# Performance work log

Measured on AMD Instinct MI355X. Metric: run time of the kernel, lower is better.

## Reference

```python
import jax, jax.numpy as jnp
import numpy as np

G = 4          # conv groups (hardcoded in module)
C = 1024       # channels (hardcoded cin=cout=1024)
SCALE = 1.0 / np.sqrt(1024.0).astype(np.float32)  # 1/sqrt(c/h), h=1


def grouped_proj(x, W, b):
    # pointwise grouped Conv1d == block-diagonal matmul over channel groups
    # x: [B, C, P], W: [G, C//G out, C//G in], b: [C]
    B, C_, P = x.shape
    xg = x.reshape(B, G, C_ // G, P)
    y = jnp.einsum('goi,bgip->bgop', W, xg)  # [B, G, C//G, P]
    return y.reshape(B, C_, P) + b[None, :, None]


def setup_inputs() -> dict:
    key = jax.random.key(0)
    ks = jax.random.split(key, 8)
    B, PK, PQ = 8, 1024, 4096
    cg = C // G
    w_std = 1.0 / np.sqrt(cg).astype(np.float32)  # ~ conv default init scale
    return {
        'Xq': jax.random.normal(ks[0], (B, C, PQ), jnp.float32),
        'Xk': jax.random.normal(ks[1], (B, C, PK), jnp.float32),
        'Wq': jax.random.normal(ks[2], (G, cg, cg), jnp.float32) * w_std,
        'bq': jax.random.normal(ks[3], (C,), jnp.float32) * 0.01,
        'Wk': jax.random.normal(ks[4], (G, cg, cg), jnp.float32) * w_std,
        'bk': jax.random.normal(ks[5], (C,), jnp.float32) * 0.01,
        'Wv': jax.random.normal(ks[6], (G, cg, cg), jnp.float32) * w_std,
        'bv': jax.random.normal(ks[7], (C,), jnp.float32) * 0.01,
    }


def reference(Xq, Xk, Wq, bq, Wk, bk, Wv, bv):
    # Q and K are both projected from Xk; V from Xq (as in the torch code)
    Q = grouped_proj(Xk, Wq, bq)   # [B, C, Pk]
    K = grouped_proj(Xk, Wk, bk)   # [B, C, Pk]
    V = grouped_proj(Xq, Wv, bv)   # [B, C, Pq]
    b, c, pk = K.shape
    pq = V.shape[-1]
    h = 1
    Qh = Q.reshape(b, h, c // h, pk)
    Kh = K.reshape(b, h, c // h, pk)
    Vh = V.reshape(b, h, c // h, pq)
    # H: [B, h, Pk, Pq], contraction over channels; softmax over dim=-2 (Pk)
    H = jnp.einsum('bhci,bhcj->bhij', Kh, Vh) * SCALE
    H = jax.nn.softmax(H, axis=-2)
    # sparse_constrain: Gram over last axis vs identity, mean squared error
    mid = jnp.einsum('bhci,bhki->bhck', H, H)          # [B, h, Pk, Pk]
    Iden = jnp.eye(pk, dtype=H.dtype)[None, None]       # broadcast over B, h
    sparse_loss = jnp.mean((mid - Iden) ** 2)
    # out: mix Q along Pk with attention H -> [B, h, C, Pq]
    out = jnp.einsum('bhij,bhki->bhkj', H, Qh).reshape(b, c, pq)
    return out, sparse_loss, H
```

## Files before the change

kernel.cpp:

```cpp
#include <hip/hip_runtime.h>

typedef _Float16 f16;
typedef f16 f16x4 __attribute__((ext_vector_type(4)));
typedef f16 f16x8 __attribute__((ext_vector_type(8)));
typedef float f32x4 __attribute__((ext_vector_type(4)));

__device__ __forceinline__ void gload16(const void* g, void* ldsbase) {
  __builtin_amdgcn_global_load_lds((const __attribute__((address_space(1))) unsigned int*)g,
                                   (__attribute__((address_space(3))) unsigned int*)ldsbase, 16, 0, 0);
}

__device__ __forceinline__ int swz(int row, int c) {
  return row * 64 + ((c ^ ((row >> 1) & 3)) << 4);
}

template<int MODE>
__global__ void __launch_bounds__(512, 2)
gemm256(const f16* __restrict__ A, const f16* __restrict__ Bm, float* __restrict__ Cf,
        f16* __restrict__ E16, f16* __restrict__ E16t,
        int K, long sA, long sB, float scale, float* __restrict__ aux) {
  __shared__ f16 sb[65536];
  const int t = threadIdx.x, l = t & 63, w = t >> 6;
  const int wr = w >> 2, wc = w & 3;
  const int bid = blockIdx.x;
  const int swzb = (bid & 7) * 64 + (bid >> 3);
  const long b = swzb >> 6;
  const int inner = swzb & 63;
  const int bx = inner >> 2, by = inner & 3;
  const char* Abyte = (const char*)(A + b * sA + (long)(by * 256) * K);
  const char* Bbyte = (const char*)(Bm + b * sB + (long)(bx * 256) * K);

  int offSrc[4];
#pragma unroll
  for (int i = 0; i < 4; ++i) {
    int cid = i * 512 + t, row = cid >> 3, slot = cid & 7;
    offSrc[i] = row * (K * 2) + ((slot ^ (row & 7)) << 4);
  }
  int offAf[8][2], offBf[4][2];
#pragma unroll
  for (int mi = 0; mi < 8; ++mi) {
    int r = wr * 128 + mi * 16 + (l & 15);
#pragma unroll
    for (int ks = 0; ks < 2; ++ks)
      offAf[mi][ks] = r * 64 + ((((ks << 2) + (l >> 4)) ^ (r & 7)) << 3);
  }
#pragma unroll
  for (int ni = 0; ni < 4; ++ni) {
    int r = wc * 64 + ni * 16 + (l & 15);
#pragma unroll
    for (int ks = 0; ks < 2; ++ks)
      offBf[ni][ks] = r * 64 + ((((ks << 2) + (l >> 4)) ^ (r & 7)) << 3);
  }

  const int NT = K >> 6;
  f32x4 acc[8][4] = {};

  auto STAGE = [&](int kt, int bsel) {
    f16* la = sb + bsel * 32768;
    f16* lb = la + 16384;
    const char* as = Abyte + (long)kt * 128;
    const char* bs = Bbyte + (long)kt * 128;
#pragma unroll
    for (int i = 0; i < 4; ++i)
      gload16(as + offSrc[i], la + (i * 512 + (w << 6)) * 8);
#pragma unroll
    for (int i = 0; i < 4; ++i)
      gload16(bs + offSrc[i], lb + (i * 512 + (w << 6)) * 8);
  };

  STAGE(0, 0);
  for (int kt = 0; kt < NT; ++kt) {
    const int cur = kt & 1;
    if (kt + 1 < NT) {
      STAGE(kt + 1, cur ^ 1);
      asm volatile("s_waitcnt vmcnt(8)" ::: "memory");
    } else {
      asm volatile("s_waitcnt vmcnt(0)" ::: "memory");
    }
    __builtin_amdgcn_s_barrier();
    asm volatile("" ::: "memory");
    const f16* la = sb + cur * 32768;
    const f16* lb = la + 16384;
#pragma unroll
    for (int ks = 0; ks < 2; ++ks) {
      f16x8 bf[4];
#pragma unroll
      for (int ni = 0; ni < 4; ++ni) bf[ni] = *(const f16x8*)(lb + offBf[ni][ks]);
#pragma unroll
      for (int mi = 0; mi < 8; ++mi) {
        f16x8 af = *(const f16x8*)(la + offAf[mi][ks]);
#pragma unroll
        for (int ni = 0; ni < 4; ++ni)
          acc[mi][ni] = __builtin_amdgcn_mfma_f32_16x16x32_f16(af, bf[ni], acc[mi][ni], 0, 0, 0);
      }
    }
    asm volatile("s_waitcnt lgkmcnt(0)" ::: "memory");
    __builtin_amdgcn_s_barrier();
    asm volatile("" ::: "memory");
  }

  const int i0 = by * 256, j0 = bx * 256;
  if (MODE == 2) {
    float csum[4] = {};
#pragma unroll
    for (int mi = 0; mi < 8; ++mi)
#pragma unroll
      for (int ni = 0; ni < 4; ++ni)
#pragma unroll
        for (int q = 0; q < 4; ++q) {
          float e = __expf(acc[mi][ni][q] * scale);
          acc[mi][ni][q] = e;
          csum[ni] += e;
        }
#pragma unroll
    for (int ni = 0; ni < 4; ++ni) {
      csum[ni] += __shfl_xor(csum[ni], 16);
      csum[ni] += __shfl_xor(csum[ni], 32);
    }
    float* colp = (float*)(sb + 34816);
    if (l < 16) {
#pragma unroll
      for (int ni = 0; ni < 4; ++ni) colp[wr * 256 + wc * 64 + ni * 16 + l] = csum[ni];
    }
    __syncthreads();
    if (t < 256) aux[(b * 4 + by) * 4096 + bx * 256 + t] = colp[t] + colp[256 + t];
    f16* E16b = E16 + b * 4194304L;
    f16* E16tb = E16t + b * 4194304L;
#pragma unroll
    for (int s = 0; s < 4; ++s) {
      if (wr == (s >> 1)) {
        const int h = s & 1;
#pragma unroll
        for (int m2 = 0; m2 < 4; ++m2)
#pragma unroll
          for (int ni = 0; ni < 4; ++ni)
#pragma unroll
            for (int q = 0; q < 4; ++q)
              sb[(m2 * 16 + (l >> 4) * 4 + q) * 264 + wc * 64 + ni * 16 + (l & 15)] =
                  (f16)acc[h * 4 + m2][ni][q];
      }
      __syncthreads();
#pragma unroll
      for (int ii = 0; ii < 4; ++ii) {
        int cid = ii * 512 + t, r = cid >> 5, cc = cid & 31;
        *(f16x8*)(E16b + (long)(i0 + s * 64 + r) * 4096 + j0 + cc * 8) =
            *(const f16x8*)(sb + r * 264 + cc * 8);
      }
      const int q4 = w >> 1, r8 = l >> 3, ic = l & 7;
#pragma unroll
      for (int ii = 0; ii < 4; ++ii) {
        int j = q4 * 64 + r8 * 8 + (w & 1) * 4 + ii;
        f16x8 v;
#pragma unroll
        for (int k2 = 0; k2 < 8; ++k2) v[k2] = sb[(ic * 8 + k2) * 264 + j];
        *(f16x8*)(E16tb + (long)(j0 + j) * 1024 + i0 + s * 64 + ic * 8) = v;
      }
      __syncthreads();
    }
  } else {
    const float* ip = aux + b * 4096 + bx * 256 + wc * 64;
    float iv[4];
#pragma unroll
    for (int ni = 0; ni < 4; ++ni) iv[ni] = ip[ni * 16 + (l & 15)];
    float* Cb = Cf + b * 4194304L + (long)(by * 256 + wr * 128) * 4096 + bx * 256 + wc * 64;
#pragma unroll
    for (int mi = 0; mi < 8; ++mi)
#pragma unroll
      for (int ni = 0; ni < 4; ++ni)
#pragma unroll
        for (int q = 0; q < 4; ++q)
          Cb[(long)(mi * 16 + (l >> 4) * 4 + q) * 4096 + ni * 16 + (l & 15)] = acc[mi][ni][q] * iv[ni];
  }
}

__global__ void __launch_bounds__(256, 2)
gram_p(const f16* __restrict__ E, const f16* __restrict__ inv2sg, float* __restrict__ parts) {
  __shared__ f16 sb[36864];
  const int t = threadIdx.x, l = t & 63, w = t >> 6, wr = w >> 1, wc = w & 1;
  const int bid = blockIdx.x;
  const int swzb = (bid & 7) * 64 + (bid >> 3);
  const long b = swzb >> 6;
  const int by = (swzb >> 3) & 7, bx = swzb & 7;
  const char* Abyte = (const char*)(E + b * 4194304L + (long)(by * 128) * 4096);
  const char* Bbyte = (const char*)(E + b * 4194304L + (long)(bx * 128) * 4096);
  f16* invl = sb + 32768;
  {
    const char* ig = (const char*)(inv2sg + b * 4096);
    gload16(ig + (long)t * 16, invl + (w << 6) * 8);
    gload16(ig + 4096 + (long)t * 16, invl + 2048 + (w << 6) * 8);
  }
  int offSrc[4];
#pragma unroll
  for (int i = 0; i < 4; ++i) {
    int cid = i * 256 + t, row = cid >> 3, slot = cid & 7;
    offSrc[i] = row * 8192 + ((slot ^ (row & 7)) << 4);
  }
  int offA[4][2], offB[4][2];
#pragma unroll
  for (int mi = 0; mi < 4; ++mi) {
    int ra = wr * 64 + mi * 16 + (l & 15);
    int rb = wc * 64 + mi * 16 + (l & 15);
#pragma unroll
    for (int ks = 0; ks < 2; ++ks) {
      offA[mi][ks] = ra * 64 + ((((ks << 2) + (l >> 4)) ^ (ra & 7)) << 3);
      offB[mi][ks] = rb * 64 + ((((ks << 2) + (l >> 4)) ^ (rb & 7)) << 3);
    }
  }
  auto STAGE = [&](int kt, int bsel) {
    f16* la = sb + bsel * 16384;
    f16* lb = la + 8192;
    const char* as = Abyte + (long)kt * 128;
    const char* bs = Bbyte + (long)kt * 128;
#pragma unroll
    for (int i = 0; i < 4; ++i) gload16(as + offSrc[i], la + (i * 256 + (w << 6)) * 8);
#pragma unroll
    for (int i = 0; i < 4; ++i) gload16(bs + offSrc[i], lb + (i * 256 + (w << 6)) * 8);
  };
  f32x4 acc[4][4] = {};
  STAGE(0, 0);
  for (int kt = 0; kt < 64; ++kt) {
    const int cur = kt & 1;
    if (kt + 1 < 64) {
      STAGE(kt + 1, cur ^ 1);
      asm volatile("s_waitcnt vmcnt(8)" ::: "memory");
    } else {
      asm volatile("s_waitcnt vmcnt(0)" ::: "memory");
    }
    __builtin_amdgcn_s_barrier();
    asm volatile("" ::: "memory");
    const f16* la = sb + cur * 16384;
    const f16* lb = la + 8192;
#pragma unroll
    for (int ks = 0; ks < 2; ++ks) {
      const f16x8 invv = *(const f16x8*)(invl + kt * 64 + ks * 32 + ((l >> 4) << 3));
      f16x8 bf[4];
#pragma unroll
      for (int ni = 0; ni < 4; ++ni) bf[ni] = *(const f16x8*)(lb + offB[ni][ks]);
#pragma unroll
      for (int mi = 0; mi < 4; ++mi) {
        f16x8 af = *(const f16x8*)(la + offA[mi][ks]) * invv;
#pragma unroll
        for (int ni = 0; ni < 4; ++ni)
          acc[mi][ni] = __builtin_amdgcn_mfma_f32_16x16x32_f16(af, bf[ni], acc[mi][ni], 0, 0, 0);
      }
    }
    asm volatile("s_waitcnt lgkmcnt(0)" ::: "memory");
    __builtin_amdgcn_s_barrier();
    asm volatile("" ::: "memory");
  }
  const int gr0 = by * 128 + wr * 64 + (l >> 4) * 4;
  const int gc0 = bx * 128 + wc * 64 + (l & 15);
  float p = 0.f;
#pragma unroll
  for (int mi = 0; mi < 4; ++mi)
#pragma unroll
    for (int ni = 0; ni < 4; ++ni)
#pragma unroll
      for (int q = 0; q < 4; ++q) {
        float e = acc[mi][ni][q] * (1.0f / 4096.0f);
        if (gr0 + mi * 16 + q == gc0 + ni * 16) e -= 1.f;
        p += e * e;
      }
#pragma unroll
  for (int d = 32; d; d >>= 1) p += __shfl_down(p, d);
  __shared__ float red[4];
  if (l == 0) red[w] = p;
  __syncthreads();
  if (t == 0) parts[bid] = red[0] + red[1] + red[2] + red[3];
}

__global__ void __launch_bounds__(512)
proj_qk(const float* __restrict__ X, const f16* __restrict__ Wq16, const f16* __restrict__ Wk16,
        const float* __restrict__ bq, const float* __restrict__ bk,
        f16* __restrict__ Q, f16* __restrict__ Kt) {
  __shared__ f16 sb[20480];
  f16* Wqs = sb;
  f16* Wks = sb + 8192;
  f16* Xs = sb + 16384;
  const int t = threadIdx.x, l = t & 63, w = t >> 6;
  const int wrq = w >> 1, wcq = w & 1;
  const int bg = blockIdx.z, g = bg & 3;
  const long b = bg >> 2;
  const int p0 = blockIdx.x * 128;
  const float* Xb = X + b * 1048576 + (long)g * 262144;
  const char* WqB = (const char*)(Wq16 + g * 65536);
  const char* WkB = (const char*)(Wk16 + g * 65536);
  int wOff[2];
#pragma unroll
  for (int i = 0; i < 2; ++i) {
    int c = i * 512 + t, row = c >> 2, slot = (c & 3) ^ ((row >> 1) & 3);
    wOff[i] = row * 512 + (slot << 4);
  }
  const int xp = t & 127, xc = t >> 7;
  const float* xS = Xb + (long)(xc * 8) * 1024 + p0 + xp;
  const int xo = swz(xp, xc);
  int offW[4], offX[4];
#pragma unroll
  for (int i = 0; i < 4; ++i) {
    int rc = wrq * 64 + i * 16 + (l & 15);
    offW[i] = swz(rc, l >> 4);
    int rp = wcq * 64 + i * 16 + (l & 15);
    offX[i] = swz(rp, l >> 4);
  }
  f32x4 accq[4][4] = {}, acck[4][4] = {};
  for (int k0 = 0; k0 < 256; k0 += 32) {
#pragma unroll
    for (int i = 0; i < 2; ++i) {
      gload16(WqB + wOff[i] + k0 * 2, Wqs + (i * 512 + (w << 6)) * 8);
      gload16(WkB + wOff[i] + k0 * 2, Wks + (i * 512 + (w << 6)) * 8);
    }
    const float* xs = xS + (long)k0 * 1024;
    f16x8 v;
#pragma unroll
    for (int d = 0; d < 8; ++d) v[d] = (f16)xs[(long)d * 1024];
    *(f16x8*)((char*)Xs + xo) = v;
    __syncthreads();
    f16x8 qf[4], kf[4], xf[4];
#pragma unroll
    for (int i = 0; i < 4; ++i) {
      qf[i] = *(const f16x8*)((const char*)Wqs + offW[i]);
      kf[i] = *(const f16x8*)((const char*)Wks + offW[i]);
      xf[i] = *(const f16x8*)((const char*)Xs + offX[i]);
    }
#pragma unroll
    for (int mi = 0; mi < 4; ++mi)
#pragma unroll
      for (int ni = 0; ni < 4; ++ni) {
        accq[mi][ni] = __builtin_amdgcn_mfma_f32_16x16x32_f16(qf[mi], xf[ni], accq[mi][ni], 0, 0, 0);
        acck[ni][mi] = __builtin_amdgcn_mfma_f32_16x16x32_f16(xf[ni], kf[mi], acck[ni][mi], 0, 0, 0);
      }
    __syncthreads();
  }
  f16* Qb = Q + b * 1048576 + (long)(g * 256 + wrq * 64) * 1024 + p0 + wcq * 64;
#pragma unroll
  for (int mi = 0; mi < 4; ++mi)
#pragma unroll
    for (int q = 0; q < 4; ++q) {
      float bv = bq[g * 256 + wrq * 64 + mi * 16 + (l >> 4) * 4 + q];
#pragma unroll
      for (int ni = 0; ni < 4; ++ni)
        Qb[(long)(mi * 16 + (l >> 4) * 4 + q) * 1024 + ni * 16 + (l & 15)] = (f16)(accq[mi][ni][q] + bv);
    }
  f16* Kb = Kt + b * 1048576 + (long)(p0 + wcq * 64) * 1024 + g * 256 + wrq * 64;
  float bcol[4];
#pragma unroll
  for (int ni = 0; ni < 4; ++ni) bcol[ni] = bk[g * 256 + wrq * 64 + ni * 16 + (l & 15)];
#pragma unroll
  for (int mi = 0; mi < 4; ++mi)
#pragma unroll
    for (int q = 0; q < 4; ++q)
#pragma unroll
      for (int ni = 0; ni < 4; ++ni)
        Kb[(long)(mi * 16 + (l >> 4) * 4 + q) * 1024 + ni * 16 + (l & 15)] = (f16)(acck[mi][ni][q] + bcol[ni]);
}

__global__ void __launch_bounds__(512)
proj_v(const float* __restrict__ X, const f16* __restrict__ Wv16, const float* __restrict__ bv,
       f16* __restrict__ Vt) {
  __shared__ f16 sb[12288];
  f16* Wvs = sb;
  f16* Xs = sb + 8192;
  const int t = threadIdx.x, l = t & 63, w = t >> 6;
  const int wrq = w >> 1, wcq = w & 1;
  const int bg = blockIdx.z, g = bg & 3;
  const long b = bg >> 2;
  const int p0 = blockIdx.x * 128;
  const float* Xb = X + b * 4194304 + (long)g * 1048576;
  const char* WvB = (const char*)(Wv16 + g * 65536);
  int wOff[2];
#pragma unroll
  for (int i = 0; i < 2; ++i) {
    int c = i * 512 + t, row = c >> 2, slot = (c & 3) ^ ((row >> 1) & 3);
    wOff[i] = row * 512 + (slot << 4);
  }
  const int xp = t & 127, xc = t >> 7;
  const float* xS = Xb + (long)(xc * 8) * 4096 + p0 + xp;
  const int xo = swz(xp, xc);
  int offW[4], offX[4];
#pragma unroll
  for (int i = 0; i < 4; ++i) {
    int rc = wrq * 64 + i * 16 + (l & 15);
    offW[i] = swz(rc, l >> 4);
    int rp = wcq * 64 + i * 16 + (l & 15);
    offX[i] = swz(rp, l >> 4);
  }
  f32x4 acc[4][4] = {};
  for (int k0 = 0; k0 < 256; k0 += 32) {
#pragma unroll
    for (int i = 0; i < 2; ++i)
      gload16(WvB + wOff[i] + k0 * 2, Wvs + (i * 512 + (w << 6)) * 8);
    const float* xs = xS + (long)k0 * 4096;
    f16x8 v;
#pragma unroll
    for (int d = 0; d < 8; ++d) v[d] = (f16)xs[(long)d * 4096];
    *(f16x8*)((char*)Xs + xo) = v;
    __syncthreads();
    f16x8 wf[4], xf[4];
#pragma unroll
    for (int i = 0; i < 4; ++i) {
      wf[i] = *(const f16x8*)((const char*)Wvs + offW[i]);
      xf[i] = *(const f16x8*)((const char*)Xs + offX[i]);
    }
#pragma unroll
    for (int mi = 0; mi < 4; ++mi)
#pragma unroll
      for (int ni = 0; ni < 4; ++ni)
        acc[mi][ni] = __builtin_amdgcn_mfma_f32_16x16x32_f16(xf[mi], wf[ni], acc[mi][ni], 0, 0, 0);
    __syncthreads();
  }
  f16* Vb = Vt + b * 4194304 + (long)(p0 + wcq * 64) * 1024 + g * 256 + wrq * 64;
  float bcol[4];
#pragma unroll
  for (int ni = 0; ni < 4; ++ni) bcol[ni] = bv[g * 256 + wrq * 64 + ni * 16 + (l & 15)];
#pragma unroll
  for (int mi = 0; mi < 4; ++mi)
#pragma unroll
    for (int q = 0; q < 4; ++q)
#pragma unroll
      for (int ni = 0; ni < 4; ++ni)
        Vb[(long)(mi * 16 + (l >> 4) * 4 + q) * 1024 + ni * 16 + (l & 15)] = (f16)(acc[mi][ni][q] + bcol[ni]);
}

__global__ void __launch_bounds__(256)
inv_k(const float* __restrict__ colsum, float* __restrict__ inv, f16* __restrict__ inv2s) {
  int gid = blockIdx.x * 256 + threadIdx.x;
  int b = gid >> 12, j = gid & 4095;
  const float* cp = colsum + (long)(b * 4) * 4096 + j;
  float s = 0.f;
#pragma unroll
  for (int my = 0; my < 4; ++my) s += cp[my * 4096];
  float iv = 1.f / s;
  inv[gid] = iv;
  inv2s[gid] = (f16)(iv * iv * 4096.0f);
}

__global__ void __launch_bounds__(256)
h_fin(const f16* __restrict__ E, float* __restrict__ Hf, const float* __restrict__ inv) {
  for (long g = blockIdx.x * 256L + threadIdx.x; g < 8388608L; g += (long)gridDim.x * 256) {
    long i4 = g * 4;
    int b = (int)(i4 >> 22), j = (int)(i4 & 4095);
    f16x4 e = *(const f16x4*)(E + i4);
    f32x4 iv = *(const f32x4*)(inv + (b << 12) + j);
    float* hp = Hf + i4;
    hp[0] = (float)e[0] * iv[0];
    hp[1] = (float)e[1] * iv[1];
    hp[2] = (float)e[2] * iv[2];
    hp[3] = (float)e[3] * iv[3];
  }
}

__global__ void cvt3(const float* __restrict__ a, const float* __restrict__ b2,
                     const float* __restrict__ c, f16* __restrict__ da,
                     f16* __restrict__ db, f16* __restrict__ dc) {
  int i = blockIdx.x * 256 + threadIdx.x;
  int which = i >> 18, r = i & 262143;
  if (which == 0) da[r] = (f16)a[r];
  else if (which == 1) db[r] = (f16)b2[r];
  else dc[r] = (f16)c[r];
}

__global__ void __launch_bounds__(256)
finalize_k(const float* __restrict__ parts, float* __restrict__ o) {
  const int t = threadIdx.x;
  float s = 0.f;
  for (int i = t; i < 512; i += 256) s += parts[i];
#pragma unroll
  for (int d = 32; d; d >>= 1) s += __shfl_down(s, d);
  __shared__ float red[4];
  if ((t & 63) == 0) red[t >> 6] = s;
  __syncthreads();
  if (t == 0) *o = (red[0] + red[1] + red[2] + red[3]) * (1.0f / 8388608.0f);
}

extern "C" void kernel_launch(void* const* d_in, const int* in_sizes, int n_in,
                              void* d_out, int out_size, void* d_ws, size_t ws_size,
                              hipStream_t stream) {
  const float* Xq = (const float*)d_in[0];
  const float* Xk = (const float*)d_in[1];
  const float* Wq = (const float*)d_in[2];
  const float* bq = (const float*)d_in[3];
  const float* Wk = (const float*)d_in[4];
  const float* bk = (const float*)d_in[5];
  const float* Wv = (const float*)d_in[6];
  const float* bv = (const float*)d_in[7];
  float* out = (float*)d_out;
  float* loss_out = out + 33554432;
  float* Hf = out + 33554433;

  char* ws = (char*)d_ws;
  f16* W16q = (f16*)(ws);
  f16* W16k = (f16*)(ws + (1 << 19));
  f16* W16v = (f16*)(ws + 2L * (1 << 19));
  f16* Q16  = (f16*)(ws + 3L * (1 << 19));
  f16* Kt16 = (f16*)(ws + 3L * (1 << 19) + (1L << 24));
  f16* Vt16 = (f16*)(ws + 3L * (1 << 19) + 2L * (1 << 24));
  f16* E16  = (f16*)(ws + 3L * (1 << 19) + 2L * (1 << 24) + (1L << 26));
  f16* E16t = (f16*)(ws + 3L * (1 << 19) + 2L * (1 << 24) + 2L * (1 << 26));
  char* tail = ws + 3L * (1 << 19) + 2L * (1 << 24) + 3L * (1 << 26);
  float* parts = (float*)tail;
  float* invb  = (float*)(tail + 8192);
  f16*   inv2s = (f16*)(tail + 8192 + 131072);
  float* colsum = (float*)(ws);

  cvt3<<<3072, 256, 0, stream>>>(Wq, Wk, Wv, W16q, W16k, W16v);

  proj_qk<<<dim3(8, 1, 32), 512, 0, stream>>>(Xk, W16q, W16k, bq, bk, Q16, Kt16);
  proj_v <<<dim3(32, 1, 32), 512, 0, stream>>>(Xq, W16v, bv, Vt16);

  gemm256<2><<<512, 512, 0, stream>>>(Kt16, Vt16, nullptr, E16, E16t,
      1024, 1L << 20, 1L << 22, 0.03125f, colsum);

  inv_k<<<128, 256, 0, stream>>>(colsum, invb, inv2s);

  gemm256<3><<<512, 512, 0, stream>>>(Q16, E16t, out, nullptr, nullptr,
      1024, 1L << 20, 1L << 22, 1.0f, invb);

  h_fin<<<2048, 256, 0, stream>>>(E16, Hf, invb);

  gram_p<<<512, 256, 0, stream>>>(E16, inv2s, parts);
  finalize_k<<<1, 256, 0, stream>>>(parts, loss_out);
}
```

Baseline: 385.1 us.

## Fuse H normalization write into gram kernel, drop separate h_fin pass

Removes the standalone h_fin kernel, which re-read the fp16 E matrix and wrote normalized fp32 H. The gram_p kernel now does this write while the matching E tile sits in LDS: blocks whose bx matches the current k-tile scale the tile by the column inverse and store it to Hf. This avoids one full read of E and one kernel launch. The cost is extra LDS reads and global stores inside the gram main loop on some iterations, which can stall the MFMA pipeline, and the write pattern (per-lane scalar stores strided by row) may be less coalesced than before.

```diff
diff --git a/kernel.cpp b/kernel.cpp
--- a/kernel.cpp
+++ b/kernel.cpp
@@ -174,8 +174,9 @@
 }
 
 __global__ void __launch_bounds__(256, 2)
-gram_p(const f16* __restrict__ E, const f16* __restrict__ inv2sg, float* __restrict__ parts) {
-  __shared__ f16 sb[36864];
+gram_p(const f16* __restrict__ E, const f16* __restrict__ inv2sg,
+       const float* __restrict__ invg, float* __restrict__ Hf, float* __restrict__ parts) {
+  __shared__ f16 sb[37888];
   const int t = threadIdx.x, l = t & 63, w = t >> 6, wr = w >> 1, wc = w & 1;
   const int bid = blockIdx.x;
   const int swzb = (bid & 7) * 64 + (bid >> 3);
@@ -184,11 +185,18 @@
   const char* Abyte = (const char*)(E + b * 4194304L + (long)(by * 128) * 4096);
   const char* Bbyte = (const char*)(E + b * 4194304L + (long)(bx * 128) * 4096);
   f16* invl = sb + 32768;
+  float* invf = (float*)(sb + 36864);
   {
     const char* ig = (const char*)(inv2sg + b * 4096);
     gload16(ig + (long)t * 16, invl + (w << 6) * 8);
     gload16(ig + 4096 + (long)t * 16, invl + 2048 + (w << 6) * 8);
   }
+  {
+    float2 v = *(const float2*)(invg + b * 4096 + bx * 512 + 2 * t);
+    invf[2 * t] = v.x;
+    invf[2 * t + 1] = v.y;
+  }
+  asm volatile("s_waitcnt lgkmcnt(0)" ::: "memory");
   int offSrc[4];
 #pragma unroll
   for (int i = 0; i < 4; ++i) {
@@ -242,6 +250,16 @@
 #pragma unroll
         for (int ni = 0; ni < 4; ++ni)
           acc[mi][ni] = __builtin_amdgcn_mfma_f32_16x16x32_f16(af, bf[ni], acc[mi][ni], 0, 0, 0);
+      }
+    }
+    if ((kt >> 3) == bx) {
+      const float iv = invf[(kt & 7) * 64 + l];
+      float* hp = Hf + b * 4194304L + (long)(by * 128) * 4096 + kt * 64 + l;
+#pragma unroll
+      for (int rr = 0; rr < 32; ++rr) {
+        const int row = w + rr * 4;
+        f16 ev = la[row * 64 + ((((l >> 3) ^ (row & 7)) << 3) | (l & 7))];
+        hp[(long)row * 4096] = (float)ev * iv;
       }
     }
     asm volatile("s_waitcnt lgkmcnt(0)" ::: "memory");
@@ -434,21 +452,6 @@
   inv2s[gid] = (f16)(iv * iv * 4096.0f);
 }
 
-__global__ void __launch_bounds__(256)
-h_fin(const f16* __restrict__ E, float* __restrict__ Hf, const float* __restrict__ inv) {
-  for (long g = blockIdx.x * 256L + threadIdx.x; g < 8388608L; g += (long)gridDim.x * 256) {
-    long i4 = g * 4;
-    int b = (int)(i4 >> 22), j = (int)(i4 & 4095);
-    f16x4 e = *(const f16x4*)(E + i4);
-    f32x4 iv = *(const f32x4*)(inv + (b << 12) + j);
-    float* hp = Hf + i4;
-    hp[0] = (float)e[0] * iv[0];
-    hp[1] = (float)e[1] * iv[1];
-    hp[2] = (float)e[2] * iv[2];
-    hp[3] = (float)e[3] * iv[3];
-  }
-}
-
 __global__ void cvt3(const float* __restrict__ a, const float* __restrict__ b2,
                      const float* __restrict__ c, f16* __restrict__ da,
                      f16* __restrict__ db, f16* __restrict__ dc) {
@@ -515,8 +518,6 @@
   gemm256<3><<<512, 512, 0, stream>>>(Q16, E16t, out, nullptr, nullptr,
       1024, 1L << 20, 1L << 22, 1.0f, invb);
 
-  h_fin<<<2048, 256, 0, stream>>>(E16, Hf, invb);
-
-  gram_p<<<512, 256, 0, stream>>>(E16, inv2s, parts);
+  gram_p<<<512, 256, 0, stream>>>(E16, inv2s, invb, Hf, parts);
   finalize_k<<<1, 256, 0, stream>>>(parts, loss_out);
 }
```

New measurement: 383.4 us. Within noise of the previous version (-0.4%).

## Deepen gram_p pipeline to four stages with half-width K tiles

Applied to the files above, without the earlier changes.

Changes the gram_p kernel's K loop from a double-buffered 64-wide tile (64 iterations) to a 4-stage ring buffer of 32-wide tiles (128 iterations), with three tiles prefetched ahead. LDS swizzle and source offsets are adjusted for the narrower rows. The intent is to hide global load latency behind MFMA work by keeping more loads in flight. In exchange it doubles the barrier count per K and gives less MFMA work per barrier.

```diff
diff --git a/kernel.cpp b/kernel.cpp
--- a/kernel.cpp
+++ b/kernel.cpp
@@ -189,60 +189,60 @@
     gload16(ig + (long)t * 16, invl + (w << 6) * 8);
     gload16(ig + 4096 + (long)t * 16, invl + 2048 + (w << 6) * 8);
   }
-  int offSrc[4];
-#pragma unroll
-  for (int i = 0; i < 4; ++i) {
-    int cid = i * 256 + t, row = cid >> 3, slot = cid & 7;
-    offSrc[i] = row * 8192 + ((slot ^ (row & 7)) << 4);
-  }
-  int offA[4][2], offB[4][2];
+  int offSrc[2];
+#pragma unroll
+  for (int i = 0; i < 2; ++i) {
+    int cid = i * 256 + t, row = cid >> 2, slot = cid & 3;
+    offSrc[i] = row * 8192 + ((slot ^ (row & 3)) << 4);
+  }
+  const int cc = l >> 4;
+  int offA[4], offB[4];
 #pragma unroll
   for (int mi = 0; mi < 4; ++mi) {
     int ra = wr * 64 + mi * 16 + (l & 15);
     int rb = wc * 64 + mi * 16 + (l & 15);
-#pragma unroll
-    for (int ks = 0; ks < 2; ++ks) {
-      offA[mi][ks] = ra * 64 + ((((ks << 2) + (l >> 4)) ^ (ra & 7)) << 3);
-      offB[mi][ks] = rb * 64 + ((((ks << 2) + (l >> 4)) ^ (rb & 7)) << 3);
-    }
+    offA[mi] = ra * 32 + ((cc ^ (ra & 3)) << 3);
+    offB[mi] = rb * 32 + ((cc ^ (rb & 3)) << 3);
   }
   auto STAGE = [&](int kt, int bsel) {
-    f16* la = sb + bsel * 16384;
-    f16* lb = la + 8192;
-    const char* as = Abyte + (long)kt * 128;
-    const char* bs = Bbyte + (long)kt * 128;
-#pragma unroll
-    for (int i = 0; i < 4; ++i) gload16(as + offSrc[i], la + (i * 256 + (w << 6)) * 8);
-#pragma unroll
-    for (int i = 0; i < 4; ++i) gload16(bs + offSrc[i], lb + (i * 256 + (w << 6)) * 8);
+    f16* la = sb + bsel * 8192;
+    f16* lb = la + 4096;
+    const char* as = Abyte + (long)kt * 64;
+    const char* bs = Bbyte + (long)kt * 64;
+#pragma unroll
+    for (int i = 0; i < 2; ++i) gload16(as + offSrc[i], la + (i * 256 + (w << 6)) * 8);
+#pragma unroll
+    for (int i = 0; i < 2; ++i) gload16(bs + offSrc[i], lb + (i * 256 + (w << 6)) * 8);
   };
   f32x4 acc[4][4] = {};
   STAGE(0, 0);
-  for (int kt = 0; kt < 64; ++kt) {
-    const int cur = kt & 1;
-    if (kt + 1 < 64) {
-      STAGE(kt + 1, cur ^ 1);
+  STAGE(1, 1);
+  STAGE(2, 2);
+  for (int kt = 0; kt < 128; ++kt) {
+    if (kt <= 124) {
+      STAGE(kt + 3, (kt + 3) & 3);
+      asm volatile("s_waitcnt vmcnt(12)" ::: "memory");
+    } else if (kt == 125) {
       asm volatile("s_waitcnt vmcnt(8)" ::: "memory");
+    } else if (kt == 126) {
+      asm volatile("s_waitcnt vmcnt(4)" ::: "memory");
     } else {
       asm volatile("s_waitcnt vmcnt(0)" ::: "memory");
     }
     __builtin_amdgcn_s_barrier();
     asm volatile("" ::: "memory");
-    const f16* la = sb + cur * 16384;
-    const f16* lb = la + 8192;
-#pragma unroll
-    for (int ks = 0; ks < 2; ++ks) {
-      const f16x8 invv = *(const f16x8*)(invl + kt * 64 + ks * 32 + ((l >> 4) << 3));
-      f16x8 bf[4];
-#pragma unroll
-      for (int ni = 0; ni < 4; ++ni) bf[ni] = *(const f16x8*)(lb + offB[ni][ks]);
-#pragma unroll
-      for (int mi = 0; mi < 4; ++mi) {
-        f16x8 af = *(const f16x8*)(la + offA[mi][ks]) * invv;
-#pragma unroll
-        for (int ni = 0; ni < 4; ++ni)
-          acc[mi][ni] = __builtin_amdgcn_mfma_f32_16x16x32_f16(af, bf[ni], acc[mi][ni], 0, 0, 0);
-      }
+    const f16* la = sb + (kt & 3) * 8192;
+    const f16* lb = la + 4096;
+    const f16x8 invv = *(const f16x8*)(invl + kt * 32 + (cc << 3));
+    f16x8 bf[4];
+#pragma unroll
+    for (int ni = 0; ni < 4; ++ni) bf[ni] = *(const f16x8*)(lb + offB[ni]);
+#pragma unroll
+    for (int mi = 0; mi < 4; ++mi) {
+      f16x8 af = *(const f16x8*)(la + offA[mi]) * invv;
+#pragma unroll
+      for (int ni = 0; ni < 4; ++ni)
+        acc[mi][ni] = __builtin_amdgcn_mfma_f32_16x16x32_f16(af, bf[ni], acc[mi][ni], 0, 0, 0);
     }
     asm volatile("s_waitcnt lgkmcnt(0)" ::: "memory");
     __builtin_amdgcn_s_barrier();
```

After: 398.4 us. +3.5%, slower.

## Fuse H output write into gram kernel and widen blocks to 512 threads

Applied to the files above, without the earlier changes.

Removes the separate h_fin pass and instead writes the fp32 H tile from the gram kernel's LDS-staged A tiles. Each block writes only the k-slices that match its bx column, so every element is written exactly once. The per-column 1/colsum factor is recovered as sqrt of the stored f16 inv^2*4096 value divided by 64. The gram kernel also goes to 8 waves with a 4x2 MFMA tile per wave, and the vmcnt waits change depending on whether the previous iteration issued stores. This saves a full re-read of E, but the precision of the recovered scale drops through the f16 square and square root, and the store traffic now sits inside the gram loop.

```diff
diff --git a/kernel.cpp b/kernel.cpp
--- a/kernel.cpp
+++ b/kernel.cpp
@@ -173,10 +173,11 @@
   }
 }
 
-__global__ void __launch_bounds__(256, 2)
-gram_p(const f16* __restrict__ E, const f16* __restrict__ inv2sg, float* __restrict__ parts) {
+__global__ void __launch_bounds__(512, 4)
+gram_p(const f16* __restrict__ E, const f16* __restrict__ inv2sg,
+       float* __restrict__ Hf, float* __restrict__ parts) {
   __shared__ f16 sb[36864];
-  const int t = threadIdx.x, l = t & 63, w = t >> 6, wr = w >> 1, wc = w & 1;
+  const int t = threadIdx.x, l = t & 63, w = t >> 6, wr = w >> 2, wc = w & 3;
   const int bid = blockIdx.x;
   const int swzb = (bid & 7) * 64 + (bid >> 3);
   const long b = swzb >> 6;
@@ -184,27 +185,27 @@
   const char* Abyte = (const char*)(E + b * 4194304L + (long)(by * 128) * 4096);
   const char* Bbyte = (const char*)(E + b * 4194304L + (long)(bx * 128) * 4096);
   f16* invl = sb + 32768;
-  {
-    const char* ig = (const char*)(inv2sg + b * 4096);
-    gload16(ig + (long)t * 16, invl + (w << 6) * 8);
-    gload16(ig + 4096 + (long)t * 16, invl + 2048 + (w << 6) * 8);
-  }
-  int offSrc[4];
-#pragma unroll
-  for (int i = 0; i < 4; ++i) {
-    int cid = i * 256 + t, row = cid >> 3, slot = cid & 7;
+  gload16((const char*)(inv2sg + b * 4096) + (long)t * 16, invl + (w << 6) * 8);
+  int offSrc[2];
+#pragma unroll
+  for (int i = 0; i < 2; ++i) {
+    int cid = i * 512 + t, row = cid >> 3, slot = cid & 7;
     offSrc[i] = row * 8192 + ((slot ^ (row & 7)) << 4);
   }
-  int offA[4][2], offB[4][2];
+  int offA[4][2], offB[2][2];
 #pragma unroll
   for (int mi = 0; mi < 4; ++mi) {
     int ra = wr * 64 + mi * 16 + (l & 15);
-    int rb = wc * 64 + mi * 16 + (l & 15);
-#pragma unroll
-    for (int ks = 0; ks < 2; ++ks) {
+#pragma unroll
+    for (int ks = 0; ks < 2; ++ks)
       offA[mi][ks] = ra * 64 + ((((ks << 2) + (l >> 4)) ^ (ra & 7)) << 3);
-      offB[mi][ks] = rb * 64 + ((((ks << 2) + (l >> 4)) ^ (rb & 7)) << 3);
-    }
+  }
+#pragma unroll
+  for (int ni = 0; ni < 2; ++ni) {
+    int rb = wc * 32 + ni * 16 + (l & 15);
+#pragma unroll
+    for (int ks = 0; ks < 2; ++ks)
+      offB[ni][ks] = rb * 64 + ((((ks << 2) + (l >> 4)) ^ (rb & 7)) << 3);
   }
   auto STAGE = [&](int kt, int bsel) {
     f16* la = sb + bsel * 16384;
@@ -212,17 +213,19 @@
     const char* as = Abyte + (long)kt * 128;
     const char* bs = Bbyte + (long)kt * 128;
 #pragma unroll
-    for (int i = 0; i < 4; ++i) gload16(as + offSrc[i], la + (i * 256 + (w << 6)) * 8);
-#pragma unroll
-    for (int i = 0; i < 4; ++i) gload16(bs + offSrc[i], lb + (i * 256 + (w << 6)) * 8);
+    for (int i = 0; i < 2; ++i) gload16(as + offSrc[i], la + (i * 512 + (w << 6)) * 8);
+#pragma unroll
+    for (int i = 0; i < 2; ++i) gload16(bs + offSrc[i], lb + (i * 512 + (w << 6)) * 8);
   };
-  f32x4 acc[4][4] = {};
+  f32x4 acc[4][2] = {};
+  const int kw0 = bx * 8;
   STAGE(0, 0);
   for (int kt = 0; kt < 64; ++kt) {
     const int cur = kt & 1;
     if (kt + 1 < 64) {
       STAGE(kt + 1, cur ^ 1);
-      asm volatile("s_waitcnt vmcnt(8)" ::: "memory");
+      if (kt - 1 >= kw0 && kt - 1 < kw0 + 8) asm volatile("s_waitcnt vmcnt(20)" ::: "memory");
+      else                                   asm volatile("s_waitcnt vmcnt(4)" ::: "memory");
     } else {
       asm volatile("s_waitcnt vmcnt(0)" ::: "memory");
     }
@@ -233,15 +236,26 @@
 #pragma unroll
     for (int ks = 0; ks < 2; ++ks) {
       const f16x8 invv = *(const f16x8*)(invl + kt * 64 + ks * 32 + ((l >> 4) << 3));
-      f16x8 bf[4];
-#pragma unroll
-      for (int ni = 0; ni < 4; ++ni) bf[ni] = *(const f16x8*)(lb + offB[ni][ks]);
+      f16x8 bf[2];
+#pragma unroll
+      for (int ni = 0; ni < 2; ++ni) bf[ni] = *(const f16x8*)(lb + offB[ni][ks]);
 #pragma unroll
       for (int mi = 0; mi < 4; ++mi) {
         f16x8 af = *(const f16x8*)(la + offA[mi][ks]) * invv;
 #pragma unroll
-        for (int ni = 0; ni < 4; ++ni)
+        for (int ni = 0; ni < 2; ++ni)
           acc[mi][ni] = __builtin_amdgcn_mfma_f32_16x16x32_f16(af, bf[ni], acc[mi][ni], 0, 0, 0);
+      }
+    }
+    if (kt >= kw0 && kt < kw0 + 8) {
+      const int jc = l;
+      const float iv = sqrtf((float)invl[kt * 64 + jc]) * (1.0f / 64.0f);
+      float* hp = Hf + b * 4194304L + (long)(by * 128 + w * 16) * 4096 + kt * 64 + jc;
+#pragma unroll
+      for (int rr = 0; rr < 16; ++rr) {
+        const int row = w * 16 + rr;
+        f16 ev = la[row * 64 + ((((jc >> 3) ^ (row & 7)) << 3) | (jc & 7))];
+        hp[(long)rr * 4096] = (float)ev * iv;
       }
     }
     asm volatile("s_waitcnt lgkmcnt(0)" ::: "memory");
@@ -249,12 +263,12 @@
     asm volatile("" ::: "memory");
   }
   const int gr0 = by * 128 + wr * 64 + (l >> 4) * 4;
-  const int gc0 = bx * 128 + wc * 64 + (l & 15);
+  const int gc0 = bx * 128 + wc * 32 + (l & 15);
   float p = 0.f;
 #pragma unroll
   for (int mi = 0; mi < 4; ++mi)
 #pragma unroll
-    for (int ni = 0; ni < 4; ++ni)
+    for (int ni = 0; ni < 2; ++ni)
 #pragma unroll
       for (int q = 0; q < 4; ++q) {
         float e = acc[mi][ni][q] * (1.0f / 4096.0f);
@@ -263,10 +277,15 @@
       }
 #pragma unroll
   for (int d = 32; d; d >>= 1) p += __shfl_down(p, d);
-  __shared__ float red[4];
+  __shared__ float red[8];
   if (l == 0) red[w] = p;
   __syncthreads();
-  if (t == 0) parts[bid] = red[0] + red[1] + red[2] + red[3];
+  if (t == 0) {
+    float s = 0.f;
+#pragma unroll
+    for (int i = 0; i < 8; ++i) s += red[i];
+    parts[bid] = s;
+  }
 }
 
 __global__ void __launch_bounds__(512)
@@ -434,21 +453,6 @@
   inv2s[gid] = (f16)(iv * iv * 4096.0f);
 }
 
-__global__ void __launch_bounds__(256)
-h_fin(const f16* __restrict__ E, float* __restrict__ Hf, const float* __restrict__ inv) {
-  for (long g = blockIdx.x * 256L + threadIdx.x; g < 8388608L; g += (long)gridDim.x * 256) {
-    long i4 = g * 4;
-    int b = (int)(i4 >> 22), j = (int)(i4 & 4095);
-    f16x4 e = *(const f16x4*)(E + i4);
-    f32x4 iv = *(const f32x4*)(inv + (b << 12) + j);
-    float* hp = Hf + i4;
-    hp[0] = (float)e[0] * iv[0];
-    hp[1] = (float)e[1] * iv[1];
-    hp[2] = (float)e[2] * iv[2];
-    hp[3] = (float)e[3] * iv[3];
-  }
-}
-
 __global__ void cvt3(const float* __restrict__ a, const float* __restrict__ b2,
                      const float* __restrict__ c, f16* __restrict__ da,
                      f16* __restrict__ db, f16* __restrict__ dc) {
@@ -515,8 +519,6 @@
   gemm256<3><<<512, 512, 0, stream>>>(Q16, E16t, out, nullptr, nullptr,
       1024, 1L << 20, 1L << 22, 1.0f, invb);
 
-  h_fin<<<2048, 256, 0, stream>>>(E16, Hf, invb);
-
-  gram_p<<<512, 256, 0, stream>>>(E16, inv2s, parts);
+  gram_p<<<512, 512, 0, stream>>>(E16, inv2s, Hf, parts);
   finalize_k<<<1, 256, 0, stream>>>(parts, loss_out);
 }
```

Measured after the change: 381.6 us. No clear change (-0.9%).
